# Performance work log

Hardware: AMD Instinct MI355X
Metric: run time of the kernel (lower is better)

The kernel has to match this reference:

```python
import math
import jax, jax.numpy as jnp
import numpy as np

TOPK = 3
NMS_K = 5
SIGMA = 3.0
TEMP = 0.07
HARD_W = 2.0
NEG_MARGIN = 0.1
NEG_INF = -1e9


def _max_pool_same(x, k):
    # torch max_pool2d(kernel=k, stride=1, padding=k//2) == SAME max reduce window
    return jax.lax.reduce_window(x, -jnp.inf, jax.lax.max, (1, 1, k, k), (1, 1, 1, 1), 'SAME')


def _extract_peaks(heatmap, topk, nms_k):
    bs, nc, H, W = heatmap.shape
    pool = _max_pool_same(heatmap, nms_k)
    nms = heatmap * (heatmap == pool).astype(heatmap.dtype)
    flat = nms.reshape(bs * nc, H * W)
    vals, idxs = jax.lax.top_k(flat, topk)
    rows = idxs // W
    cols = idxs % W
    coords = jnp.stack([rows, cols], -1).reshape(bs, nc, topk, 2)
    return coords, vals.reshape(bs, nc, topk), idxs.reshape(bs, nc, topk)


def _bilinear_sample(fm, rows, cols):
    # fm (V,C,H,W); rows/cols (V,K) float pixel coords (align_corners=True round-trip)
    V, C, H, W = fm.shape
    y0 = jnp.floor(rows); x0 = jnp.floor(cols)
    wy = rows - y0; wx = cols - x0
    y0i = jnp.clip(y0.astype(jnp.int32), 0, H - 1)
    y1i = jnp.clip(y0i + 1, 0, H - 1)
    x0i = jnp.clip(x0.astype(jnp.int32), 0, W - 1)
    x1i = jnp.clip(x0i + 1, 0, W - 1)

    def one(f, a0, a1, b0, b1, vy, vx):
        v00 = f[:, a0, b0]; v01 = f[:, a0, b1]  # (C,K)
        v10 = f[:, a1, b0]; v11 = f[:, a1, b1]
        top = v00 * (1 - vx) + v01 * vx
        bot = v10 * (1 - vx) + v11 * vx
        return top * (1 - vy) + bot * vy

    return jax.vmap(one)(fm, y0i, y1i, x0i, x1i, wy, wx)  # (V,C,K)


def _forward(heatmap, feature_map, phase_embed, W1, b1, W2, b2, logit_scale,
             phase_embeds, next_targets, pos_mask, neg_mask, hard_neg_mask):
    bs, nc, H, W = heatmap.shape
    V = feature_map.shape[0]

    # --- PeakExtractor: maxpool NMS + topk ---
    peak_coords, _, _ = _extract_peaks(heatmap, TOPK, NMS_K)
    coords0 = peak_coords[0].astype(jnp.float32)  # (V,K,2)

    # --- PhaseConditionedPeakSelector: grid_sample (align_corners=True) + MLP + cosine logits ---
    sampled = _bilinear_sample(feature_map, coords0[..., 0], coords0[..., 1])  # (V,C,K)
    sampled = sampled.transpose(0, 2, 1)  # (V,K,C)
    h = jnp.maximum(sampled @ W1 + b1, 0.0)
    pe = h @ W2 + b2
    pe = pe / jnp.maximum(jnp.linalg.norm(pe, axis=-1, keepdims=True), 1e-12)
    scale = jnp.minimum(jnp.exp(logit_scale[0]), 100.0)
    peak_logits = jnp.einsum('vkd,d->vk', pe, phase_embed[0]) * scale  # (V,K)

    # --- reweight_heatmap_with_peaks: gaussian bias bumps at peaks ---
    w = jax.nn.softmax(peak_logits, axis=-1)  # (V,K)
    rr = jnp.arange(H, dtype=jnp.float32)
    cc = jnp.arange(W, dtype=jnp.float32)
    dr = rr[None, None, :, None] - coords0[..., 0][:, :, None, None]  # (V,K,H,1)
    dc = cc[None, None, None, :] - coords0[..., 1][:, :, None, None]  # (V,K,1,W)
    gauss = jnp.exp(-(dr * dr + dc * dc) / (2.0 * SIGMA * SIGMA))      # (V,K,H,W)
    bias = jnp.einsum('vk,vkhw->vhw', w, gauss)                        # (V,H,W)
    reweighted = heatmap[:, :, None] + bias[None, :, None]             # (bs,nc,1,H,W)

    # --- contrastive_phase_loss ---
    sim = (phase_embeds @ phase_embeds.T) / TEMP
    pos_sim = jnp.where(pos_mask, sim, NEG_INF)
    lse_pos = jax.nn.logsumexp(pos_sim, axis=-1)
    neg_logits = jnp.where(neg_mask, sim, NEG_INF) + hard_neg_mask.astype(sim.dtype) * math.log(HARD_W)
    lse_neg = jax.nn.logsumexp(neg_logits, axis=-1)
    log_denom = jnp.logaddexp(lse_pos, lse_neg)
    valid = pos_mask.any(axis=-1)
    per_anchor = -(lse_pos - log_denom)
    c_loss = jnp.sum(jnp.where(valid, per_anchor, 0.0)) / jnp.maximum(valid.sum(), 1).astype(sim.dtype)

    # --- phase_consistency_loss ---
    a, b = phase_embeds[:-1], phase_embeds[1:]
    cos = jnp.sum(a * b, -1) / jnp.maximum(
        jnp.linalg.norm(a, axis=-1) * jnp.linalg.norm(b, axis=-1), 1e-8)
    tdiff = jnp.linalg.norm(next_targets[:-1] - next_targets[1:], axis=-1)
    same = (tdiff < NEG_MARGIN).astype(cos.dtype)
    cons_loss = jnp.mean(same * jnp.maximum(same * 0.9 - cos, 0.0))

    return reweighted, peak_logits, c_loss, cons_loss


def setup_inputs() -> dict:
    key = jax.random.key(0)
    ks = jax.random.split(key, 12)
    bs, nc, H, W = 4, 5, 512, 512
    V, C, D, N = 5, 128, 64, 2048
    heatmap = jax.random.normal(ks[0], (bs, nc, H, W), jnp.float32)
    feature_map = jax.random.normal(ks[1], (V, C, H, W), jnp.float32)
    phase_embed = jax.random.normal(ks[2], (1, D), jnp.float32)
    phase_embed = phase_embed / jnp.linalg.norm(phase_embed, axis=-1, keepdims=True)
    W1 = jax.random.normal(ks[3], (C, D), jnp.float32) * 0.05
    b1 = jnp.zeros((D,), jnp.float32)
    W2 = jax.random.normal(ks[4], (D, D), jnp.float32) * 0.05
    b2 = jnp.zeros((D,), jnp.float32)
    logit_scale = jnp.full((1,), math.log(1.0 / 0.07), jnp.float32)
    pe = jax.random.normal(ks[5], (N, D), jnp.float32)
    phase_embeds = pe / jnp.linalg.norm(pe, axis=-1, keepdims=True)
    next_targets = jax.random.normal(ks[6], (N, 3), jnp.float32) * 0.05
    eye = jnp.eye(N, dtype=bool)
    pos_mask = (jax.random.uniform(ks[7], (N, N)) < 0.02) & ~eye
    neg_mask = ~pos_mask & ~eye
    hard_neg_mask = neg_mask & (jax.random.uniform(ks[8], (N, N)) < 0.05)
    return {"heatmap": heatmap, "feature_map": feature_map, "phase_embed": phase_embed,
            "W1": W1, "b1": b1, "W2": W2, "b2": b2, "logit_scale": logit_scale,
            "phase_embeds": phase_embeds, "next_targets": next_targets,
            "pos_mask": pos_mask, "neg_mask": neg_mask, "hard_neg_mask": hard_neg_mask}


def reference(heatmap, feature_map, phase_embed, W1, b1, W2, b2, logit_scale,
              phase_embeds, next_targets, pos_mask, neg_mask, hard_neg_mask):
    return _forward(heatmap, feature_map, phase_embed, W1, b1, W2, b2, logit_scale,
                    phase_embeds, next_targets, pos_mask, neg_mask, hard_neg_mask)
```

## Files before the change

kernel.cpp:

```cpp
#include <hip/hip_runtime.h>
#include <float.h>
#include <limits.h>

typedef float4 f4;

#define HH 512
#define WW 512
#define NC 5
#define NBS 4
#define CF 128
#define DD 64
#define NN 2048
#define HW 262144
#define OUT_RW 5242880
#define LN2F 0.6931471805599453f
#define INV_TEMP 14.285714285714286f

#define WS_PEAKS  64
#define WS_WSOFT  192
#define WS_BTV    256
#define WS_BTI    15616
#define WS_RLOSS  31232
#define WS_RVALID 39424
#define WS_CONS   47616
#define WS_PMM    49152
#define WS_PMS    (WS_PMM + 262144)
#define WS_NMM    (WS_PMS + 262144)
#define WS_NMS    (WS_NMM + 262144)

#define BETTER(v1,i1,v2,i2) ((v1) > (v2) || ((v1) == (v2) && (i1) < (i2)))
#define DOT4(a,b) ((a).x*(b).x + (a).y*(b).y + (a).z*(b).z + (a).w*(b).w)

__device__ __forceinline__ void merge3(float&a0,float&a1,float&a2,int&ai0,int&ai1,int&ai2,
                                       float b0,float b1,float b2,int bi0,int bi1,int bi2){
  float c0=a0,c1=a1,c2=a2; int ci0=ai0,ci1=ai1,ci2=ai2;
  float x0,x1,x2; int y0,y1,y2;
  if (BETTER(c0,ci0,b0,bi0)){ x0=c0;y0=ci0; c0=c1;ci0=ci1; c1=c2;ci1=ci2; c2=-FLT_MAX; ci2=INT_MAX; }
  else { x0=b0;y0=bi0; b0=b1;bi0=bi1; b1=b2;bi1=bi2; b2=-FLT_MAX; bi2=INT_MAX; }
  if (BETTER(c0,ci0,b0,bi0)){ x1=c0;y1=ci0; c0=c1;ci0=ci1; }
  else { x1=b0;y1=bi0; b0=b1;bi0=bi1; }
  if (BETTER(c0,ci0,b0,bi0)){ x2=c0;y2=ci0; }
  else { x2=b0;y2=bi0; }
  a0=x0;a1=x1;a2=x2; ai0=y0;ai1=y1;ai2=y2;
}

__global__ __launch_bounds__(256) void ka_nms_sim(const float* __restrict__ heat,
    float* __restrict__ btv, int* __restrict__ bti,
    const float* __restrict__ E,
    const void* __restrict__ pm, const void* __restrict__ nm, const void* __restrict__ hm,
    float* __restrict__ pmm, float* __restrict__ pms,
    float* __restrict__ nmm_, float* __restrict__ nms_){
  __shared__ f4 As[64*17];
  __shared__ f4 Bs[64*16];
  int blk = blockIdx.x;
  int t = threadIdx.x;

  if (blk < 1280){
    float* svf = (float*)As;
    int*   sii = ((int*)As) + 768;
    int c = blk >> 8, s = blk & 255;
    const float* Hc = heat + c * HW;
    float v0=-FLT_MAX, v1=-FLT_MAX, v2=-FLT_MAX;
    int   i0=INT_MAX,  i1=INT_MAX,  i2=INT_MAX;
    int base = s * 1024;
    #pragma unroll
    for (int k = 0; k < 4; ++k){
      int p = base + t + 256*k;
      int r = p >> 9, col = p & 511;
      float v = Hc[p];
      float m = v;
      #pragma unroll
      for (int dr = -2; dr <= 2; ++dr){
        int rr = r + dr;
        if ((unsigned)rr >= (unsigned)HH) continue;
        const float* Hr = Hc + (rr << 9);
        #pragma unroll
        for (int dc = -2; dc <= 2; ++dc){
          int c2 = col + dc;
          if ((unsigned)c2 >= (unsigned)WW) continue;
          m = fmaxf(m, Hr[c2]);
        }
      }
      float nv = (v == m) ? v : 0.0f;
      if (BETTER(nv, p, v2, i2)){
        if (BETTER(nv, p, v0, i0)){ v2=v1;i2=i1; v1=v0;i1=i0; v0=nv;i0=p; }
        else if (BETTER(nv, p, v1, i1)){ v2=v1;i2=i1; v1=nv;i1=p; }
        else { v2=nv; i2=p; }
      }
    }
    svf[t*3+0]=v0; svf[t*3+1]=v1; svf[t*3+2]=v2;
    sii[t*3+0]=i0; sii[t*3+1]=i1; sii[t*3+2]=i2;
    for (int off = 128; off; off >>= 1){
      __syncthreads();
      if (t < off){
        float a0=svf[t*3], a1=svf[t*3+1], a2=svf[t*3+2];
        int   ai0=sii[t*3], ai1=sii[t*3+1], ai2=sii[t*3+2];
        int u = t + off;
        merge3(a0,a1,a2,ai0,ai1,ai2,
               svf[u*3],svf[u*3+1],svf[u*3+2], sii[u*3],sii[u*3+1],sii[u*3+2]);
        svf[t*3]=a0; svf[t*3+1]=a1; svf[t*3+2]=a2;
        sii[t*3]=ai0; sii[t*3+1]=ai1; sii[t*3+2]=ai2;
      }
    }
    if (t == 0){
      int o = blk * 3;
      btv[o]=svf[0]; btv[o+1]=svf[1]; btv[o+2]=svf[2];
      bti[o]=sii[0]; bti[o+1]=sii[1]; bti[o+2]=sii[2];
    }
    return;
  }

  int sb = blk - 1280;
  int bc = sb & 31, br = sb >> 5;
  int R0 = br * 64, C0 = bc * 64;
  unsigned int wdet = ((const unsigned int*)nm)[t & 63];
  unsigned long long bal = __ballot(wdet > 1u && wdet != 0x3F800000u);
  int mode = (bal != 0ull) ? 2 : 0;

  const f4* E4 = (const f4*)E;
  #pragma unroll
  for (int k = 0; k < 4; ++k){
    int f = t + 256*k;
    int rr = f >> 4, dc = f & 15;
    As[rr*17 + dc] = E4[(R0 + rr)*16 + dc];
    Bs[rr*16 + (dc ^ (rr >> 2))] = E4[(C0 + rr)*16 + dc];
  }
  __syncthreads();
  int tx = t & 15, ty = t >> 4;
  float acc[4][4] = {};
  #pragma unroll 4
  for (int dc = 0; dc < 16; ++dc){
    f4 a0 = As[(ty*4+0)*17 + dc];
    f4 a1 = As[(ty*4+1)*17 + dc];
    f4 a2 = As[(ty*4+2)*17 + dc];
    f4 a3 = As[(ty*4+3)*17 + dc];
    #pragma unroll
    for (int j = 0; j < 4; ++j){
      f4 b = Bs[(tx*4+j)*16 + (dc ^ tx)];
      acc[0][j] += DOT4(a0,b);
      acc[1][j] += DOT4(a1,b);
      acc[2][j] += DOT4(a2,b);
      acc[3][j] += DOT4(a3,b);
    }
  }
  int cbase = C0 + tx*4;
  #pragma unroll
  for (int ri = 0; ri < 4; ++ri){
    int row = R0 + ty*4 + ri;
    int ofs = row * NN + cbase;
    bool p0,p1,p2,p3, n0,n1,n2,n3, h0,h1,h2,h3;
    if (mode != 2){
      int4 a = *(const int4*)((const int*)pm + ofs);
      int4 bq = *(const int4*)((const int*)nm + ofs);
      int4 cq = *(const int4*)((const int*)hm + ofs);
      p0=a.x!=0; p1=a.y!=0; p2=a.z!=0; p3=a.w!=0;
      n0=bq.x!=0; n1=bq.y!=0; n2=bq.z!=0; n3=bq.w!=0;
      h0=cq.x!=0; h1=cq.y!=0; h2=cq.z!=0; h3=cq.w!=0;
    } else {
      unsigned int a = *(const unsigned int*)((const unsigned char*)pm + ofs);
      unsigned int bq = *(const unsigned int*)((const unsigned char*)nm + ofs);
      unsigned int cq = *(const unsigned int*)((const unsigned char*)hm + ofs);
      p0=(a&0xffu)!=0; p1=(a&0xff00u)!=0; p2=(a&0xff0000u)!=0; p3=(a&0xff000000u)!=0;
      n0=(bq&0xffu)!=0; n1=(bq&0xff00u)!=0; n2=(bq&0xff0000u)!=0; n3=(bq&0xff000000u)!=0;
      h0=(cq&0xffu)!=0; h1=(cq&0xff00u)!=0; h2=(cq&0xff0000u)!=0; h3=(cq&0xff000000u)!=0;
    }
    float s0 = acc[ri][0]*INV_TEMP, s1 = acc[ri][1]*INV_TEMP,
          s2 = acc[ri][2]*INV_TEMP, s3 = acc[ri][3]*INV_TEMP;
    float xp0 = p0 ? s0 : -1e9f, xp1 = p1 ? s1 : -1e9f,
          xp2 = p2 ? s2 : -1e9f, xp3 = p3 ? s3 : -1e9f;
    float xn0 = (n0 ? s0 : -1e9f) + (h0 ? LN2F : 0.f);
    float xn1 = (n1 ? s1 : -1e9f) + (h1 ? LN2F : 0.f);
    float xn2 = (n2 ? s2 : -1e9f) + (h2 ? LN2F : 0.f);
    float xn3 = (n3 ? s3 : -1e9f) + (h3 ? LN2F : 0.f);
    float mp = fmaxf(fmaxf(xp0,xp1), fmaxf(xp2,xp3));
    float mn = fmaxf(fmaxf(xn0,xn1), fmaxf(xn2,xn3));
    #pragma unroll
    for (int off = 1; off < 16; off <<= 1){
      mp = fmaxf(mp, __shfl_xor(mp, off));
      mn = fmaxf(mn, __shfl_xor(mn, off));
    }
    float sp = __expf(xp0-mp) + __expf(xp1-mp) + __expf(xp2-mp) + __expf(xp3-mp);
    float sn = __expf(xn0-mn) + __expf(xn1-mn) + __expf(xn2-mn) + __expf(xn3-mn);
    #pragma unroll
    for (int off = 1; off < 16; off <<= 1){
      sp += __shfl_xor(sp, off);
      sn += __shfl_xor(sn, off);
    }
    if (tx == 0){
      pmm [bc*NN + row] = mp;  pms [bc*NN + row] = sp;
      nmm_[bc*NN + row] = mn;  nms_[bc*NN + row] = sn;
    }
  }
}

__global__ __launch_bounds__(1024) void km2(
    const float* __restrict__ btv, const int* __restrict__ bti,
    const float* __restrict__ fm,
    const float* __restrict__ W1, const float* __restrict__ b1,
    const float* __restrict__ W2, const float* __restrict__ b2,
    const float* __restrict__ pemb, const float* __restrict__ lsc,
    const float* __restrict__ pmm, const float* __restrict__ pms,
    const float* __restrict__ nmm_, const float* __restrict__ nms_,
    const float* __restrict__ E, const float* __restrict__ T,
    int* __restrict__ peaks, float* __restrict__ wsoft,
    float* __restrict__ rloss, int* __restrict__ rvalid, float* __restrict__ consp,
    float* __restrict__ out){
  int blk = blockIdx.x;
  int t = threadIdx.x;

  if (blk == 0){
    __shared__ int pk[30];
    __shared__ float logits[15];
    __shared__ float samp[15][CF];
    __shared__ float hbuf[15][DD];
    int wave = t >> 6, lane = t & 63;
    if (wave < 5){
      int ch = wave;
      int e0 = ch*768 + lane*3;
      float v0=btv[e0], v1=btv[e0+1], v2=btv[e0+2];
      int   i0=bti[e0], i1=bti[e0+1], i2=bti[e0+2];
      #pragma unroll
      for (int s = 1; s < 4; ++s){
        int e = ch*768 + (lane + s*64)*3;
        merge3(v0,v1,v2,i0,i1,i2, btv[e],btv[e+1],btv[e+2], bti[e],bti[e+1],bti[e+2]);
      }
      #pragma unroll
      for (int off = 32; off; off >>= 1){
        float b0=__shfl_xor(v0,off), b1=__shfl_xor(v1,off), b2=__shfl_xor(v2,off);
        int   j0=__shfl_xor(i0,off), j1=__shfl_xor(i1,off), j2=__shfl_xor(i2,off);
        merge3(v0,v1,v2,i0,i1,i2, b0,b1,b2, j0,j1,j2);
      }
      if (lane == 0){
        pk[ch*6+0]=i0>>9; pk[ch*6+1]=i0&511;
        pk[ch*6+2]=i1>>9; pk[ch*6+3]=i1&511;
        pk[ch*6+4]=i2>>9; pk[ch*6+5]=i2&511;
        #pragma unroll
        for (int q = 0; q < 6; ++q) peaks[ch*6+q] = pk[ch*6+q];
      }
    }
    __syncthreads();
    for (int u = t; u < 15*CF; u += 1024){
      int vk = u >> 7, chn = u & 127;
      int v = vk / 3;
      int r = pk[vk*2], cc = pk[vk*2+1];
      samp[vk][chn] = fm[((v*CF + chn) << 18) + (r << 9) + cc];
    }
    __syncthreads();
    if (t < 15*DD){
      int vk = t >> 6, d = t & 63;
      float acc = b1[d];
      #pragma unroll 4
      for (int chn = 0; chn < CF; ++chn) acc += samp[vk][chn] * W1[chn*DD + d];
      hbuf[vk][d] = fmaxf(acc, 0.0f);
    }
    __syncthreads();
    {
      int vk = t >> 6, d = t & 63;
      if (vk < 15){
        float acc = b2[d];
        #pragma unroll 4
        for (int e = 0; e < DD; ++e) acc += hbuf[vk][e] * W2[e*DD + d];
        float ss = acc * acc;
        #pragma unroll
        for (int off = 32; off; off >>= 1) ss += __shfl_xor(ss, off);
        float inv = 1.0f / fmaxf(sqrtf(ss), 1e-12f);
        float contrib = (acc * inv) * pemb[d];
        #pragma unroll
        for (int off = 32; off; off >>= 1) contrib += __shfl_xor(contrib, off);
        if (d == 0){
          float scale = fminf(__expf(lsc[0]), 100.0f);
          logits[vk] = contrib * scale;
        }
      }
    }
    __syncthreads();
    if (t < 5){
      int v = t;
      float l0 = logits[v*3], l1 = logits[v*3+1], l2 = logits[v*3+2];
      float mm = fmaxf(l0, fmaxf(l1, l2));
      float e0 = __expf(l0-mm), e1 = __expf(l1-mm), e2 = __expf(l2-mm);
      float sm = e0 + e1 + e2;
      wsoft[v*3] = e0/sm; wsoft[v*3+1] = e1/sm; wsoft[v*3+2] = e2/sm;
      out[OUT_RW + v*3 + 0] = l0;
      out[OUT_RW + v*3 + 1] = l1;
      out[OUT_RW + v*3 + 2] = l2;
    }
    return;
  }

  int r = (blk - 1) * 1024 + t;
  float mp = pmm[r];
  #pragma unroll 8
  for (int k = 1; k < 32; ++k) mp = fmaxf(mp, pmm[k*NN + r]);
  float sp = 0.f;
  #pragma unroll 8
  for (int k = 0; k < 32; ++k) sp += pms[k*NN + r] * __expf(pmm[k*NN + r] - mp);
  float mn = nmm_[r];
  #pragma unroll 8
  for (int k = 1; k < 32; ++k) mn = fmaxf(mn, nmm_[k*NN + r]);
  float sn = 0.f;
  #pragma unroll 8
  for (int k = 0; k < 32; ++k) sn += nms_[k*NN + r] * __expf(nmm_[k*NN + r] - mn);
  float lp = mp + __logf(sp), ln = mn + __logf(sn);
  float mm = fmaxf(lp, ln);
  float ld = mm + __logf(__expf(lp - mm) + __expf(ln - mm));
  bool valid = mp > -1e8f;
  rloss[r]  = valid ? (ld - lp) : 0.f;
  rvalid[r] = valid ? 1 : 0;
  float cs = 0.f;
  if (r < NN - 1){
    const f4* a4 = (const f4*)(E + r*DD);
    const f4* b4 = (const f4*)(E + (r+1)*DD);
    float dot=0.f, na=0.f, nb=0.f;
    #pragma unroll
    for (int q = 0; q < 16; ++q){
      f4 a = a4[q], b = b4[q];
      dot += DOT4(a,b); na += DOT4(a,a); nb += DOT4(b,b);
    }
    float cosv = dot / fmaxf(sqrtf(na)*sqrtf(nb), 1e-8f);
    float t0 = T[r*3]   - T[r*3+3];
    float t1 = T[r*3+1] - T[r*3+4];
    float t2 = T[r*3+2] - T[r*3+5];
    float td = sqrtf(t0*t0 + t1*t1 + t2*t2);
    if (td < 0.1f) cs = fmaxf(0.9f - cosv, 0.f);
  }
  __shared__ float red[1024];
  red[t] = cs;
  __syncthreads();
  for (int off = 512; off; off >>= 1){
    if (t < off) red[t] += red[t + off];
    __syncthreads();
  }
  if (t == 0) consp[blk - 1] = red[0];
}

__global__ __launch_bounds__(256) void k3f_rwfin(const float* __restrict__ heat,
    const int* __restrict__ peaks, const float* __restrict__ wsoft,
    const float* __restrict__ rloss, const int* __restrict__ rvalid,
    const float* __restrict__ consp,
    float* __restrict__ out){
  int blk = blockIdx.x;
  int t = threadIdx.x;

  if (blk < 1280){
    __shared__ float pr[3], pc[3], w3[3];
    int gid = blk * 256 + t;
    int c = gid >> 16;
    if (t < 3){
      pr[t] = (float)peaks[c*6 + t*2];
      pc[t] = (float)peaks[c*6 + t*2 + 1];
      w3[t] = wsoft[c*3 + t];
    }
    __syncthreads();
    int rem = (gid & 65535) << 2;
    int h = rem >> 9, x0 = rem & 511;
    float bias0=0.f, bias1=0.f, bias2=0.f, bias3=0.f;
    #pragma unroll
    for (int k = 0; k < 3; ++k){
      float dr = (float)h - pr[k];
      float dr2 = dr*dr;
      float w = w3[k];
      float d0 = (float)x0     - pc[k];
      float d1 = (float)(x0+1) - pc[k];
      float d2 = (float)(x0+2) - pc[k];
      float d3 = (float)(x0+3) - pc[k];
      float q0 = dr2 + d0*d0, q1 = dr2 + d1*d1, q2 = dr2 + d2*d2, q3 = dr2 + d3*d3;
      if (q0 < 324.f) bias0 += w * __expf(-q0 * (1.0f/18.0f));
      if (q1 < 324.f) bias1 += w * __expf(-q1 * (1.0f/18.0f));
      if (q2 < 324.f) bias2 += w * __expf(-q2 * (1.0f/18.0f));
      if (q3 < 324.f) bias3 += w * __expf(-q3 * (1.0f/18.0f));
    }
    #pragma unroll
    for (int b = 0; b < NBS; ++b){
      int idx = ((b*NC + c) << 18) + rem;
      f4 hv = *(const f4*)(heat + idx);
      f4 o; o.x = hv.x + bias0; o.y = hv.y + bias1; o.z = hv.z + bias2; o.w = hv.w + bias3;
      *(f4*)(out + idx) = o;
    }
    return;
  }

  float s = 0.f; int cnt = 0;
  #pragma unroll
  for (int i = t; i < NN; i += 256){ s += rloss[i]; cnt += rvalid[i]; }
  float cs = (t < 2) ? consp[t] : 0.f;
  __shared__ float r1[256]; __shared__ int r2[256]; __shared__ float r3[256];
  r1[t] = s; r2[t] = cnt; r3[t] = cs;
  __syncthreads();
  for (int off = 128; off; off >>= 1){
    if (t < off){ r1[t] += r1[t+off]; r2[t] += r2[t+off]; r3[t] += r3[t+off]; }
    __syncthreads();
  }
  if (t == 0){
    int c = r2[0] > 1 ? r2[0] : 1;
    out[OUT_RW + 15] = r1[0] / (float)c;
    out[OUT_RW + 16] = r3[0] / (float)(NN - 1);
  }
}

extern "C" void kernel_launch(void* const* d_in, const int* in_sizes, int n_in,
                              void* d_out, int out_size, void* d_ws, size_t ws_size,
                              hipStream_t stream) {
  (void)in_sizes; (void)n_in; (void)out_size; (void)ws_size;
  const float* heat = (const float*)d_in[0];
  const float* fm   = (const float*)d_in[1];
  const float* pemb = (const float*)d_in[2];
  const float* W1   = (const float*)d_in[3];
  const float* b1   = (const float*)d_in[4];
  const float* W2   = (const float*)d_in[5];
  const float* b2   = (const float*)d_in[6];
  const float* lsc  = (const float*)d_in[7];
  const float* E    = (const float*)d_in[8];
  const float* T    = (const float*)d_in[9];
  const void*  pm   = d_in[10];
  const void*  nmm  = d_in[11];
  const void*  hmm  = d_in[12];
  float* out = (float*)d_out;
  char* ws = (char*)d_ws;
  int*   peaks  = (int*)(ws + WS_PEAKS);
  float* wsoft  = (float*)(ws + WS_WSOFT);
  float* btv    = (float*)(ws + WS_BTV);
  int*   bti    = (int*)(ws + WS_BTI);
  float* rloss  = (float*)(ws + WS_RLOSS);
  int*   rvalid = (int*)(ws + WS_RVALID);
  float* consp  = (float*)(ws + WS_CONS);
  float* pmm    = (float*)(ws + WS_PMM);
  float* pms    = (float*)(ws + WS_PMS);
  float* nmm2   = (float*)(ws + WS_NMM);
  float* nms2   = (float*)(ws + WS_NMS);

  hipLaunchKernelGGL(ka_nms_sim, dim3(2304), dim3(256),  0, stream,
                     heat, btv, bti, E, pm, nmm, hmm, pmm, pms, nmm2, nms2);
  hipLaunchKernelGGL(km2,        dim3(3),    dim3(1024), 0, stream,
                     btv, bti, fm, W1, b1, W2, b2, pemb, lsc,
                     pmm, pms, nmm2, nms2, E, T,
                     peaks, wsoft, rloss, rvalid, consp, out);
  hipLaunchKernelGGL(k3f_rwfin,  dim3(1281), dim3(256),  0, stream,
                     heat, peaks, wsoft, rloss, rvalid, consp, out);
}
```

Baseline: 81.62 us.

## Stage heatmap rows in shared memory and use separable 5x5 max pooling

The NMS blocks now load a 6-row halo tile of the heatmap into shared memory, compute vertical 5-tap column maxima into a padded buffer, then take horizontal 5-tap maxima. This replaces the 25 global loads per pixel with one cooperative load plus shared-memory reads, cutting redundant global traffic and branching. It adds two barriers and uses about 24 KB of shared memory, which could reduce occupancy.

```diff
diff --git a/kernel.cpp b/kernel.cpp
--- a/kernel.cpp
+++ b/kernel.cpp
@@ -56,38 +56,60 @@
   int t = threadIdx.x;
 
   if (blk < 1280){
+    float* rowbuf = (float*)As;
+    float* colmax = (float*)Bs;
+    int c = blk >> 8, s = blk & 255;
+    const float* Hc = heat + c * HW;
+
+    for (int i = t; i < 3072; i += 256){
+      int rowi = i >> 9, cc = i & 511;
+      int grow = 2*s - 2 + rowi;
+      rowbuf[i] = ((unsigned)grow < (unsigned)HH) ? Hc[(grow << 9) + cc] : -FLT_MAX;
+    }
+    if (t < 8){
+      int rl = t >> 2, q = t & 3;
+      colmax[rl*516 + (q < 2 ? q : 512 + q)] = -FLT_MAX;
+    }
+    __syncthreads();
+
+    #pragma unroll
+    for (int k = 0; k < 4; ++k){
+      int p = t + 256*k;
+      int rl = p >> 9, cc = p & 511;
+      float cm =          rowbuf[(rl+0)*512 + cc];
+      cm = fmaxf(cm,      rowbuf[(rl+1)*512 + cc]);
+      cm = fmaxf(cm,      rowbuf[(rl+2)*512 + cc]);
+      cm = fmaxf(cm,      rowbuf[(rl+3)*512 + cc]);
+      cm = fmaxf(cm,      rowbuf[(rl+4)*512 + cc]);
+      colmax[rl*516 + 2 + cc] = cm;
+    }
+    __syncthreads();
+
+    float v0=-FLT_MAX, v1=-FLT_MAX, v2=-FLT_MAX;
+    int   i0=INT_MAX,  i1=INT_MAX,  i2=INT_MAX;
+    #pragma unroll
+    for (int k = 0; k < 4; ++k){
+      int p = t + 256*k;
+      int rl = p >> 9, cc = p & 511;
+      float v = rowbuf[(rl+2)*512 + cc];
+      int b5 = rl*516 + 2 + cc;
+      float m =          colmax[b5-2];
+      m = fmaxf(m,       colmax[b5-1]);
+      m = fmaxf(m,       colmax[b5  ]);
+      m = fmaxf(m,       colmax[b5+1]);
+      m = fmaxf(m,       colmax[b5+2]);
+      float nv = (v == m) ? v : 0.0f;
+      int pidx = s*1024 + p;
+      if (BETTER(nv, pidx, v2, i2)){
+        if (BETTER(nv, pidx, v0, i0)){ v2=v1;i2=i1; v1=v0;i1=i0; v0=nv;i0=pidx; }
+        else if (BETTER(nv, pidx, v1, i1)){ v2=v1;i2=i1; v1=nv;i1=pidx; }
+        else { v2=nv; i2=pidx; }
+      }
+    }
+    __syncthreads();
+
     float* svf = (float*)As;
     int*   sii = ((int*)As) + 768;
-    int c = blk >> 8, s = blk & 255;
-    const float* Hc = heat + c * HW;
-    float v0=-FLT_MAX, v1=-FLT_MAX, v2=-FLT_MAX;
-    int   i0=INT_MAX,  i1=INT_MAX,  i2=INT_MAX;
-    int base = s * 1024;
-    #pragma unroll
-    for (int k = 0; k < 4; ++k){
-      int p = base + t + 256*k;
-      int r = p >> 9, col = p & 511;
-      float v = Hc[p];
-      float m = v;
-      #pragma unroll
-      for (int dr = -2; dr <= 2; ++dr){
-        int rr = r + dr;
-        if ((unsigned)rr >= (unsigned)HH) continue;
-        const float* Hr = Hc + (rr << 9);
-        #pragma unroll
-        for (int dc = -2; dc <= 2; ++dc){
-          int c2 = col + dc;
-          if ((unsigned)c2 >= (unsigned)WW) continue;
-          m = fmaxf(m, Hr[c2]);
-        }
-      }
-      float nv = (v == m) ? v : 0.0f;
-      if (BETTER(nv, p, v2, i2)){
-        if (BETTER(nv, p, v0, i0)){ v2=v1;i2=i1; v1=v0;i1=i0; v0=nv;i0=p; }
-        else if (BETTER(nv, p, v1, i1)){ v2=v1;i2=i1; v1=nv;i1=p; }
-        else { v2=nv; i2=p; }
-      }
-    }
     svf[t*3+0]=v0; svf[t*3+1]=v1; svf[t*3+2]=v2;
     sii[t*3+0]=i0; sii[t*3+1]=i1; sii[t*3+2]=i2;
     for (int off = 128; off; off >>= 1){
```

Result: faster. 67.54 us (-17.3%).
